# Performance work log

Hardware: AMD Instinct MI355X
Metric: run time of the kernel (lower is better)

## Reference

```python
import jax, jax.numpy as jnp
import numpy as np
import math

NO, NR, E = 100000, 1000, 1000000
DO, DR, DE, H, OM = 64, 32, 4, 64, 32


def setup_inputs() -> dict:
    key = jax.random.key(0)
    ks = jax.random.split(key, 20)
    s = lambda k, sh: jax.random.normal(k, sh, dtype=jnp.float32) * 0.05
    inp = {
        'x_order': jax.random.normal(ks[0], (NO, DO), dtype=jnp.float32),
        'x_rider': jax.random.normal(ks[1], (NR, DR), dtype=jnp.float32),
        'edge_attr': jax.random.normal(ks[2], (E, DE), dtype=jnp.float32),
        'order_idx': jax.random.randint(ks[3], (E,), 0, NO),
        'rider_idx': jax.random.randint(ks[4], (E,), 0, NR),
        'omega_encoded': jax.random.normal(ks[5], (OM,), dtype=jnp.float32),
        # TransformerConv params (heads=1)
        'Wk': s(ks[6], (DO, H)), 'bk': jnp.zeros((H,), jnp.float32),
        'Wq': s(ks[7], (DR, H)), 'bq': jnp.zeros((H,), jnp.float32),
        'Wv': s(ks[8], (DO, H)), 'bv': jnp.zeros((H,), jnp.float32),
        'We': s(ks[9], (DE, H)),  # lin_edge, bias=False in PyG
        'Wskip': s(ks[10], (DR, H)), 'bskip': jnp.zeros((H,), jnp.float32),
        # order_proj
        'Wp': s(ks[11], (DO, H)), 'bp': jnp.zeros((H,), jnp.float32),
        # residual MLP: Linear(2H+OM,128) -> ReLU -> Linear(128,1)
        'W1': s(ks[12], (2 * H + OM, 128)), 'b1': jnp.zeros((128,), jnp.float32),
        'W2': s(ks[13], (128, 1)), 'b2': jnp.zeros((1,), jnp.float32),
    }
    return inp


def _segment_softmax(alpha, seg, num_segments):
    m = jax.ops.segment_max(alpha, seg, num_segments=num_segments)
    m = jnp.where(jnp.isfinite(m), m, 0.0)
    ex = jnp.exp(alpha - m[seg])
    denom = jax.ops.segment_sum(ex, seg, num_segments=num_segments)
    return ex / (denom[seg] + 1e-16)


def reference(x_order, x_rider, edge_attr, order_idx, rider_idx, omega_encoded,
              Wk, bk, Wq, bq, Wv, bv, We, Wskip, bskip, Wp, bp, W1, b1, W2, b2):
    scale = 1.0 / math.sqrt(H)
    # TransformerConv((order, rider) -> rider), heads=1, edge_dim
    q = x_rider @ Wq + bq            # [NR, H]
    k = x_order @ Wk + bk            # [NO, H]
    v = x_order @ Wv + bv            # [NO, H]
    e = edge_attr @ We               # [E, H]
    k_j = k[order_idx] + e           # [E, H]
    v_j = v[order_idx] + e           # [E, H]
    alpha = jnp.sum(q[rider_idx] * k_j, axis=-1) * scale  # [E]
    alpha = _segment_softmax(alpha, rider_idx, NR)
    agg = jax.ops.segment_sum(alpha[:, None] * v_j, rider_idx, num_segments=NR)  # [NR, H]
    rider_emb = agg + x_rider @ Wskip + bskip  # root/skip connection

    # edge scoring
    order_proj = x_order @ Wp + bp   # [NO, H]
    oe = order_proj[order_idx]       # [E, H]
    re = rider_emb[rider_idx]        # [E, H]
    dot = jnp.sum(oe * re, axis=-1) * scale  # [E]
    omega_expand = jnp.broadcast_to(omega_encoded[None, :], (oe.shape[0], OM))
    resid_in = jnp.concatenate([oe, re, omega_expand], axis=-1)  # [E, 2H+OM]
    hmid = jax.nn.relu(resid_in @ W1 + b1)
    resid = (hmid @ W2 + b2)[:, 0]
    return jnp.clip(dot + resid, -10.0, 10.0)
```

## Files before the change

kernel.cpp:

```cpp
#include <hip/hip_runtime.h>
#include <hip/hip_bf16.h>
#include <math.h>

#define NO_N 100000
#define NR_N 1000
#define E_N  1000000
#define SB     250
#define SCHUNK 4000
#define KVP_TILES 1563
#define KVP_BLKS 521
#define MAXTILES 17008

typedef short bf16x8 __attribute__((ext_vector_type(8)));
typedef float floatx4 __attribute__((ext_vector_type(4)));

__device__ __forceinline__ unsigned short bfu(float x) {
    union { __hip_bfloat16 h; unsigned short u; } c;
    c.h = __float2bfloat16(x);
    return c.u;
}
__device__ __forceinline__ float bflo(unsigned int u) {
    return __uint_as_float(u << 16);
}
__device__ __forceinline__ float bfhi(unsigned int u) {
    return __uint_as_float(u & 0xffff0000u);
}

__global__ __launch_bounds__(256) void k_front(
    const float* __restrict__ xr,
    const float* __restrict__ Wq, const float* __restrict__ bq,
    const float* __restrict__ Wskip, const float* __restrict__ bskip,
    const float* __restrict__ We,
    float* __restrict__ q, float* __restrict__ skip, float* __restrict__ t,
    const float* __restrict__ W1, const float* __restrict__ b1,
    const float* __restrict__ omega, float* __restrict__ b1eff,
    const float* __restrict__ x,
    const float* __restrict__ Wk, const float* __restrict__ bk,
    const float* __restrict__ Wv, const float* __restrict__ bv,
    const float* __restrict__ Wp, const float* __restrict__ bp,
    unsigned short* __restrict__ kb, unsigned short* __restrict__ vb,
    unsigned short* __restrict__ pb,
    const int* __restrict__ ridx, int* __restrict__ ghist)
{
    __shared__ __align__(16) char smem[9216];
    const int tid = threadIdx.x;
    const int b = blockIdx.x;

    if (b < 250) {
        float* sx = (float*)smem;
        float* sq = sx + 128;
        int rbase = b * 4;
        if (tid < 128) {
            int rl = tid >> 5, d = tid & 31;
            sx[rl * 32 + d] = xr[(rbase + rl) * 32 + d];
        }
        __syncthreads();
        int rl = tid >> 6, h = tid & 63;
        int r = rbase + rl;
        float aq = bq[h], as = bskip[h];
        #pragma unroll 4
        for (int d = 0; d < 32; ++d) {
            float xv = sx[rl * 32 + d];
            aq += xv * Wq[d * 64 + h];
            as += xv * Wskip[d * 64 + h];
        }
        sq[rl * 64 + h] = aq;
        q[r * 64 + h] = aq;
        skip[r * 64 + h] = as;
        __syncthreads();
        if (tid < 16) {
            int rl2 = tid >> 2, d = tid & 3;
            float acc = 0.f;
            for (int hh = 0; hh < 64; ++hh)
                acc += We[d * 64 + hh] * sq[rl2 * 64 + hh];
            t[(rbase + rl2) * 4 + d] = acc;
        }
    } else if (b == 250) {
        if (tid < 128) {
            float acc = b1[tid];
            #pragma unroll 4
            for (int j = 0; j < 32; ++j)
                acc += omega[j] * W1[(128 + j) * 128 + tid];
            b1eff[tid] = acc;
        }
    } else if (b < 251 + KVP_BLKS) {
        unsigned short* sX = (unsigned short*)smem;
        const int wave = tid >> 6, lane = tid & 63;
        const int l15 = lane & 15, quad = lane >> 4;

        bf16x8 bfr[3][2];
        float bias[3];
        unsigned short* outT[3];
        int colc[3];
        #pragma unroll
        for (int ct = 0; ct < 3; ++ct) {
            int n = wave * 48 + ct * 16 + l15;
            int table = n >> 6, c = n & 63;
            const float* W  = (table == 0) ? Wk : (table == 1) ? Wv : Wp;
            const float* bb = (table == 0) ? bk : (table == 1) ? bv : bp;
            bias[ct] = bb[c];
            colc[ct] = c;
            outT[ct] = (table == 0) ? kb : (table == 1) ? vb : pb;
            #pragma unroll
            for (int kf = 0; kf < 2; ++kf) {
                bf16x8 f;
                #pragma unroll
                for (int j = 0; j < 8; ++j)
                    f[j] = (short)bfu(W[(size_t)(kf * 32 + quad * 8 + j) * 64 + c]);
                bfr[ct][kf] = f;
            }
        }

        const int srl = tid >> 2;
        const int sqt = (tid & 3) * 16;

        for (int tile = b - 251; tile < KVP_TILES; tile += KVP_BLKS) {
            int rowbase = tile * 64;
            {
                int row = rowbase + srl;
                unsigned short* dst = sX + srl * 72 + sqt;
                if (row < NO_N) {
                    const float4* src = (const float4*)(x + (size_t)row * 64 + sqt);
                    #pragma unroll
                    for (int i = 0; i < 4; ++i) {
                        float4 a = src[i];
                        ushort4 u = { bfu(a.x), bfu(a.y), bfu(a.z), bfu(a.w) };
                        *(ushort4*)(dst + i * 4) = u;
                    }
                } else {
                    ushort4 z = {0, 0, 0, 0};
                    #pragma unroll
                    for (int i = 0; i < 4; ++i) *(ushort4*)(dst + i * 4) = z;
                }
            }
            __syncthreads();

            floatx4 acc[4][3];
            #pragma unroll
            for (int rt = 0; rt < 4; ++rt)
                #pragma unroll
                for (int ct = 0; ct < 3; ++ct)
                    acc[rt][ct] = (floatx4){bias[ct], bias[ct], bias[ct], bias[ct]};

            #pragma unroll
            for (int rt = 0; rt < 4; ++rt) {
                const unsigned short* ar = sX + (size_t)(rt * 16 + l15) * 72 + quad * 8;
                bf16x8 a0 = *(const bf16x8*)(ar);
                bf16x8 a1 = *(const bf16x8*)(ar + 32);
                #pragma unroll
                for (int ct = 0; ct < 3; ++ct) {
                    floatx4 c = acc[rt][ct];
                    c = __builtin_amdgcn_mfma_f32_16x16x32_bf16(a0, bfr[ct][0], c, 0, 0, 0);
                    c = __builtin_amdgcn_mfma_f32_16x16x32_bf16(a1, bfr[ct][1], c, 0, 0, 0);
                    acc[rt][ct] = c;
                }
            }

            #pragma unroll
            for (int rt = 0; rt < 4; ++rt) {
                int rb = rowbase + rt * 16 + quad * 4;
                #pragma unroll
                for (int ct = 0; ct < 3; ++ct) {
                    unsigned short* o = outT[ct];
                    size_t cbase = colc[ct];
                    #pragma unroll
                    for (int g = 0; g < 4; ++g) {
                        int row = rb + g;
                        if (row < NO_N)
                            o[(size_t)row * 64 + cbase] = bfu(acc[rt][ct][g]);
                    }
                }
            }
            __syncthreads();
        }
    } else {
        int* hc = (int*)smem;
        int hb = b - (251 + KVP_BLKS);
        for (int i = tid; i < NR_N; i += 256) hc[i] = 0;
        __syncthreads();
        int s = hb * SCHUNK;
        for (int i = s + tid; i < s + SCHUNK; i += 256)
            atomicAdd(&hc[ridx[i]], 1);
        __syncthreads();
        for (int i = tid; i < NR_N; i += 256)
            ghist[i * SB + hb] = hc[i];
    }
}

__global__ __launch_bounds__(256) void k_colscan(const int* __restrict__ ghist,
                                                 int* __restrict__ gpre,
                                                 int* __restrict__ counts)
{
    __shared__ int s[256];
    int tid = threadIdx.x, r = blockIdx.x;
    int v = (tid < SB) ? ghist[r * SB + tid] : 0;
    s[tid] = v;
    __syncthreads();
    for (int off = 1; off < 256; off <<= 1) {
        int tv = (tid >= off) ? s[tid - off] : 0;
        __syncthreads();
        s[tid] += tv;
        __syncthreads();
    }
    if (tid < SB) gpre[r * SB + tid] = s[tid] - v;
    if (tid == 255) counts[r] = s[255];
}

__global__ __launch_bounds__(1024) void k_scan(const int* __restrict__ counts,
                                               int* __restrict__ offsets,
                                               int* __restrict__ tilestart,
                                               int* __restrict__ tile2r)
{
    __shared__ int s[1024];
    int tid = threadIdx.x;
    int c = (tid < NR_N) ? counts[tid] : 0;
    s[tid] = c;
    __syncthreads();
    for (int off = 1; off < 1024; off <<= 1) {
        int tv = (tid >= off) ? s[tid - off] : 0;
        __syncthreads();
        s[tid] += tv;
        __syncthreads();
    }
    if (tid < NR_N) offsets[tid] = s[tid] - c;
    if (tid == NR_N - 1) offsets[NR_N] = s[tid];
    __syncthreads();
    int tc = (tid < NR_N) ? ((c + 63) >> 6) : 0;
    s[tid] = tc;
    __syncthreads();
    for (int off = 1; off < 1024; off <<= 1) {
        int tv = (tid >= off) ? s[tid - off] : 0;
        __syncthreads();
        s[tid] += tv;
        __syncthreads();
    }
    if (tid < NR_N) {
        int ts = s[tid] - tc;
        tilestart[tid] = ts;
        for (int t = 0; t < tc; ++t) tile2r[ts + t] = tid;
    }
    if (tid == NR_N - 1) tilestart[NR_N] = s[tid];
}

__global__ __launch_bounds__(256) void k_scatter2(
    const int* __restrict__ ridx, const int* __restrict__ oidx,
    const float* __restrict__ ea, const float* __restrict__ t,
    const int* __restrict__ offsets, const int* __restrict__ gpre,
    int4* __restrict__ spack, int* __restrict__ so, int* __restrict__ rank)
{
    __shared__ int cur[NR_N];
    int tid = threadIdx.x, b = blockIdx.x;
    for (int i = tid; i < NR_N; i += 256)
        cur[i] = offsets[i] + gpre[i * SB + b];
    __syncthreads();
    int s = b * SCHUNK;
    for (int i = s + tid; i < s + SCHUNK; i += 256) {
        int r = ridx[i];
        int o = oidx[i];
        float4 e4 = *(const float4*)(ea + (size_t)i * 4);
        float4 t4 = *(const float4*)(t + r * 4);
        float h = e4.x * t4.x + e4.y * t4.y + e4.z * t4.z + e4.w * t4.w;
        int pos = atomicAdd(&cur[r], 1);
        int4 pk;
        pk.x = o;
        pk.y = __float_as_int(h);
        pk.z = (int)((unsigned)bfu(e4.x) | ((unsigned)bfu(e4.y) << 16));
        pk.w = (int)((unsigned)bfu(e4.z) | ((unsigned)bfu(e4.w) << 16));
        spack[pos] = pk;
        so[pos] = o;
        rank[i] = pos;
    }
}

__global__ __launch_bounds__(1024) void k_rider(
    const int* __restrict__ offsets, const int4* __restrict__ spack,
    const float* __restrict__ q,
    const unsigned short* __restrict__ kb, const unsigned short* __restrict__ vb,
    const float* __restrict__ We, const float* __restrict__ skip,
    const float* __restrict__ W1, const float* __restrict__ b1eff,
    float* __restrict__ emb, float* __restrict__ Br)
{
    __shared__ float sQ[64];
    __shared__ int2 sOX[16][64];
    __shared__ float rv[16][64];
    __shared__ float re4[16][4];
    __shared__ float rd[16];

    int r = blockIdx.x;
    int wave = threadIdx.x >> 6, lane = threadIdx.x & 63;
    if (threadIdx.x < 64) sQ[threadIdx.x] = q[r * 64 + threadIdx.x];
    __syncthreads();

    int beg = offsets[r], end = offsets[r + 1];
    int cnt = end - beg;
    int chunk = (cnt + 15) >> 4;
    int s0 = beg + wave * chunk;
    int s1 = min(s0 + chunk, end);

    float aggv = 0.f, dsum = 0.f;
    float ag0 = 0.f, ag1 = 0.f, ag2 = 0.f, ag3 = 0.f;
    const float2* sQ2 = (const float2*)sQ;

    for (int jb = s0; jb < s1; jb += 64) {
        int j = jb + lane;
        bool valid = (j < s1);
        int4 pk = make_int4(0, 0, 0, 0);
        if (valid) pk = spack[j];
        int oo = pk.x;
        float h = __int_as_float(pk.y);

        const uint4* krow = (const uint4*)(kb + (size_t)oo * 64);
        uint4 K0 = krow[0], K1 = krow[1], K2 = krow[2], K3 = krow[3];
        uint4 K4 = krow[4], K5 = krow[5], K6 = krow[6], K7 = krow[7];
        float acc = h;
        #define DOT8(Kv, base) { \
            float2 qa = sQ2[(base) + 0]; \
            acc = fmaf(bflo(Kv.x), qa.x, acc); acc = fmaf(bfhi(Kv.x), qa.y, acc); \
            float2 qb = sQ2[(base) + 1]; \
            acc = fmaf(bflo(Kv.y), qb.x, acc); acc = fmaf(bfhi(Kv.y), qb.y, acc); \
            float2 qc = sQ2[(base) + 2]; \
            acc = fmaf(bflo(Kv.z), qc.x, acc); acc = fmaf(bfhi(Kv.z), qc.y, acc); \
            float2 qd = sQ2[(base) + 3]; \
            acc = fmaf(bflo(Kv.w), qd.x, acc); acc = fmaf(bfhi(Kv.w), qd.y, acc); }
        DOT8(K0, 0) DOT8(K1, 4) DOT8(K2, 8) DOT8(K3, 12)
        DOT8(K4, 16) DOT8(K5, 20) DOT8(K6, 24) DOT8(K7, 28)
        #undef DOT8

        float exv = valid ? __expf(acc * 0.125f) : 0.f;
        dsum += exv;
        unsigned int ez = (unsigned int)pk.z, ew = (unsigned int)pk.w;
        ag0 = fmaf(exv, bflo(ez), ag0);
        ag1 = fmaf(exv, bfhi(ez), ag1);
        ag2 = fmaf(exv, bflo(ew), ag2);
        ag3 = fmaf(exv, bfhi(ew), ag3);

        sOX[wave][lane] = make_int2(oo, __float_as_int(exv));

        int nn = min(s1 - jb, 64);
        int i = 0;
        for (; i + 8 <= nn; i += 8) {
            int2 x0 = sOX[wave][i + 0], x1 = sOX[wave][i + 1];
            int2 x2 = sOX[wave][i + 2], x3 = sOX[wave][i + 3];
            int2 x4 = sOX[wave][i + 4], x5 = sOX[wave][i + 5];
            int2 x6 = sOX[wave][i + 6], x7 = sOX[wave][i + 7];
            unsigned short u0 = vb[(size_t)x0.x * 64 + lane];
            unsigned short u1 = vb[(size_t)x1.x * 64 + lane];
            unsigned short u2 = vb[(size_t)x2.x * 64 + lane];
            unsigned short u3 = vb[(size_t)x3.x * 64 + lane];
            unsigned short u4 = vb[(size_t)x4.x * 64 + lane];
            unsigned short u5 = vb[(size_t)x5.x * 64 + lane];
            unsigned short u6 = vb[(size_t)x6.x * 64 + lane];
            unsigned short u7 = vb[(size_t)x7.x * 64 + lane];
            aggv = fmaf(__int_as_float(x0.y), __uint_as_float((unsigned int)u0 << 16), aggv);
            aggv = fmaf(__int_as_float(x1.y), __uint_as_float((unsigned int)u1 << 16), aggv);
            aggv = fmaf(__int_as_float(x2.y), __uint_as_float((unsigned int)u2 << 16), aggv);
            aggv = fmaf(__int_as_float(x3.y), __uint_as_float((unsigned int)u3 << 16), aggv);
            aggv = fmaf(__int_as_float(x4.y), __uint_as_float((unsigned int)u4 << 16), aggv);
            aggv = fmaf(__int_as_float(x5.y), __uint_as_float((unsigned int)u5 << 16), aggv);
            aggv = fmaf(__int_as_float(x6.y), __uint_as_float((unsigned int)u6 << 16), aggv);
            aggv = fmaf(__int_as_float(x7.y), __uint_as_float((unsigned int)u7 << 16), aggv);
        }
        for (; i < nn; ++i) {
            int2 xx = sOX[wave][i];
            unsigned short uu = vb[(size_t)xx.x * 64 + lane];
            aggv = fmaf(__int_as_float(xx.y), __uint_as_float((unsigned int)uu << 16), aggv);
        }
    }

    #pragma unroll
    for (int m = 1; m < 64; m <<= 1) {
        dsum += __shfl_xor(dsum, m);
        ag0 += __shfl_xor(ag0, m);
        ag1 += __shfl_xor(ag1, m);
        ag2 += __shfl_xor(ag2, m);
        ag3 += __shfl_xor(ag3, m);
    }

    rv[wave][lane] = aggv;
    if (lane == 0) {
        rd[wave] = dsum;
        re4[wave][0] = ag0; re4[wave][1] = ag1;
        re4[wave][2] = ag2; re4[wave][3] = ag3;
    }
    __syncthreads();
    if (threadIdx.x < 64) {
        int l = threadIdx.x;
        float av = 0.f, ds = 0.f, a0 = 0.f, a1 = 0.f, a2 = 0.f, a3 = 0.f;
        #pragma unroll 4
        for (int w = 0; w < 16; ++w) {
            av += rv[w][l]; ds += rd[w];
            a0 += re4[w][0]; a1 += re4[w][1]; a2 += re4[w][2]; a3 += re4[w][3];
        }
        float corr = a0 * We[0 * 64 + l] + a1 * We[1 * 64 + l]
                   + a2 * We[2 * 64 + l] + a3 * We[3 * 64 + l];
        float val = (av + corr) / (ds + 1e-16f) + skip[r * 64 + l];
        emb[r * 64 + l] = val;
        sQ[l] = val;
    }
    __syncthreads();
    if (threadIdx.x < 128) {
        int c = threadIdx.x;
        float a = b1eff[c];
        #pragma unroll 8
        for (int d = 0; d < 64; ++d)
            a = fmaf(sQ[d], W1[(size_t)(64 + d) * 128 + c], a);
        Br[r * 128 + c] = a;
    }
}

__global__ __launch_bounds__(256, 3) void k_edge2(
    const int* __restrict__ so, const int* __restrict__ offsets,
    const int* __restrict__ tilestart, const int* __restrict__ tile2r,
    const unsigned short* __restrict__ pb, const float* __restrict__ emb,
    const float* __restrict__ Br, const float* __restrict__ W1,
    const float* __restrict__ W2, const float* __restrict__ b2,
    float* __restrict__ tmp)
{
    __shared__ __align__(16) unsigned short sA[64 * 72];
    __shared__ float sDot[64];

    const int tid = threadIdx.x;
    const int wave = tid >> 6;
    const int lane = tid & 63;
    const int l15 = lane & 15;
    const int quad = lane >> 4;

    bf16x8 bfr[8][2];
    float w2v[8];
    #pragma unroll
    for (int ctl = 0; ctl < 8; ++ctl) {
        int n = ctl * 16 + l15;
        w2v[ctl] = W2[n];
        #pragma unroll
        for (int kc = 0; kc < 2; ++kc) {
            bf16x8 f;
            #pragma unroll
            for (int j = 0; j < 8; ++j)
                f[j] = (short)bfu(W1[(size_t)(kc * 32 + quad * 8 + j) * 128 + n]);
            bfr[ctl][kc] = f;
        }
    }
    float b2v = b2[0];
    const int ntiles = tilestart[NR_N];

    const int el = tid >> 2;
    const int q16 = (tid & 3) * 16;

    for (int tile = blockIdx.x; tile < ntiles; tile += gridDim.x) {
        int r = tile2r[tile];
        int jb = offsets[r] + ((tile - tilestart[r]) << 6);
        int jend = offsets[r + 1];

        {
            int j = jb + el;
            int o = so[min(j, jend - 1)];
            const uint4* po = (const uint4*)(pb + (size_t)o * 64 + q16);
            uint4 A0 = po[0], A1 = po[1];
            const float4* pe = (const float4*)(emb + r * 64 + q16);
            float4 e0 = pe[0], e1 = pe[1], e2 = pe[2], e3 = pe[3];
            float dotp;
            dotp  = bflo(A0.x) * e0.x + bfhi(A0.x) * e0.y;
            dotp += bflo(A0.y) * e0.z + bfhi(A0.y) * e0.w;
            dotp += bflo(A0.z) * e1.x + bfhi(A0.z) * e1.y;
            dotp += bflo(A0.w) * e1.z + bfhi(A0.w) * e1.w;
            dotp += bflo(A1.x) * e2.x + bfhi(A1.x) * e2.y;
            dotp += bflo(A1.y) * e2.z + bfhi(A1.y) * e2.w;
            dotp += bflo(A1.z) * e3.x + bfhi(A1.z) * e3.y;
            dotp += bflo(A1.w) * e3.z + bfhi(A1.w) * e3.w;
            uint4* sp = (uint4*)(sA + el * 72 + q16);
            sp[0] = A0; sp[1] = A1;
            dotp += __shfl_xor(dotp, 1);
            dotp += __shfl_xor(dotp, 2);
            if ((tid & 3) == 0) sDot[el] = dotp;
        }

        const unsigned short* ar = sA + (size_t)(wave * 16 + l15) * 72 + quad * 8;
        bf16x8 a0 = *(const bf16x8*)(ar);
        bf16x8 a1 = *(const bf16x8*)(ar + 32);
        floatx4 acc[8];
        #pragma unroll
        for (int ctl = 0; ctl < 8; ++ctl) {
            floatx4 c = (floatx4){0.f, 0.f, 0.f, 0.f};
            c = __builtin_amdgcn_mfma_f32_16x16x32_bf16(a0, bfr[ctl][0], c, 0, 0, 0);
            c = __builtin_amdgcn_mfma_f32_16x16x32_bf16(a1, bfr[ctl][1], c, 0, 0, 0);
            acc[ctl] = c;
        }

        float brv[8];
        #pragma unroll
        for (int ctl = 0; ctl < 8; ++ctl)
            brv[ctl] = Br[r * 128 + ctl * 16 + l15];

        floatx4 s;
        #pragma unroll
        for (int g = 0; g < 4; ++g) {
            float v = 0.f;
            #pragma unroll
            for (int ctl = 0; ctl < 8; ++ctl)
                v = fmaf(fmaxf(acc[ctl][g] + brv[ctl], 0.f), w2v[ctl], v);
            s[g] = v;
        }
        #pragma unroll
        for (int m = 1; m < 16; m <<= 1) {
            s[0] += __shfl_xor(s[0], m);
            s[1] += __shfl_xor(s[1], m);
            s[2] += __shfl_xor(s[2], m);
            s[3] += __shfl_xor(s[3], m);
        }
        if (l15 == 0) {
            int rowb = wave * 16 + quad * 4;
            #pragma unroll
            for (int g = 0; g < 4; ++g) {
                int pos = jb + rowb + g;
                if (pos < jend) {
                    float v = s[g] + 0.125f * sDot[rowb + g] + b2v;
                    tmp[pos] = fminf(fmaxf(v, -10.f), 10.f);
                }
            }
        }
    }
}

__global__ __launch_bounds__(256) void k_perm(const int* __restrict__ rank,
                                              const float* __restrict__ tmp,
                                              float* __restrict__ out)
{
    int i = blockIdx.x * 256 + threadIdx.x;
    if (i < E_N) out[i] = tmp[rank[i]];
}

extern "C" void kernel_launch(void* const* d_in, const int* in_sizes, int n_in,
                              void* d_out, int out_size, void* d_ws, size_t ws_size,
                              hipStream_t stream)
{
    const float* x_order   = (const float*)d_in[0];
    const float* x_rider   = (const float*)d_in[1];
    const float* edge_attr = (const float*)d_in[2];
    const int*   order_idx = (const int*)d_in[3];
    const int*   rider_idx = (const int*)d_in[4];
    const float* omega     = (const float*)d_in[5];
    const float* Wk = (const float*)d_in[6];  const float* bk = (const float*)d_in[7];
    const float* Wq = (const float*)d_in[8];  const float* bq = (const float*)d_in[9];
    const float* Wv = (const float*)d_in[10]; const float* bv = (const float*)d_in[11];
    const float* We = (const float*)d_in[12];
    const float* Wskip = (const float*)d_in[13]; const float* bskip = (const float*)d_in[14];
    const float* Wp = (const float*)d_in[15]; const float* bp = (const float*)d_in[16];
    const float* W1 = (const float*)d_in[17]; const float* b1 = (const float*)d_in[18];
    const float* W2 = (const float*)d_in[19]; const float* b2 = (const float*)d_in[20];
    float* out = (float*)d_out;

    unsigned short* ws_kb = (unsigned short*)d_ws;
    unsigned short* ws_vb = ws_kb + (size_t)NO_N * 64;
    unsigned short* ws_pb = ws_vb + (size_t)NO_N * 64;
    int4* ws_spack = (int4*)(ws_pb + (size_t)NO_N * 64);
    float* ws_tmp  = (float*)ws_spack;
    int*  ws_so    = (int*)(ws_spack + E_N);
    int*  ws_rank  = ws_so + E_N;
    float* wsf     = (float*)(ws_rank + E_N);
    float* ws_q    = wsf;
    float* ws_skip = ws_q + NR_N * 64;
    float* ws_emb  = ws_skip + NR_N * 64;
    float* ws_t    = ws_emb + NR_N * 64;
    float* ws_b1e  = ws_t + NR_N * 4;
    float* ws_Br   = ws_b1e + 128;
    int* ws_counts  = (int*)(ws_Br + NR_N * 128);
    int* ws_offsets = ws_counts + NR_N;
    int* ws_tilest  = ws_offsets + NR_N + 8;
    int* ws_tile2r  = ws_tilest + NR_N + 8;
    int* ws_ghist   = ws_tile2r + MAXTILES;
    int* ws_gpre    = ws_ghist + NR_N * SB;

    k_front<<<251 + KVP_BLKS + SB, 256, 0, stream>>>(
        x_rider, Wq, bq, Wskip, bskip, We, ws_q, ws_skip, ws_t,
        W1, b1, omega, ws_b1e,
        x_order, Wk, bk, Wv, bv, Wp, bp, ws_kb, ws_vb, ws_pb,
        rider_idx, ws_ghist);
    k_colscan<<<NR_N, 256, 0, stream>>>(ws_ghist, ws_gpre, ws_counts);
    k_scan<<<1, 1024, 0, stream>>>(ws_counts, ws_offsets, ws_tilest, ws_tile2r);
    k_scatter2<<<SB, 256, 0, stream>>>(rider_idx, order_idx, edge_attr, ws_t,
                                       ws_offsets, ws_gpre, ws_spack, ws_so, ws_rank);
    k_rider<<<NR_N, 1024, 0, stream>>>(ws_offsets, ws_spack, ws_q,
                                       ws_kb, ws_vb, We, ws_skip,
                                       W1, ws_b1e, ws_emb, ws_Br);
    k_edge2<<<2048, 256, 0, stream>>>(ws_so, ws_offsets, ws_tilest, ws_tile2r,
                                      ws_pb, ws_emb, ws_Br, W1, W2, b2, ws_tmp);
    k_perm<<<(E_N + 255) / 256, 256, 0, stream>>>(ws_rank, ws_tmp, out);
}
```

Measured before the change: 312.6 us.

## Prefetch next edge tile's gathers in k_edge2 and use contiguous tile ranges

k_edge2 now gives each block a contiguous range of tiles instead of a grid-strided loop. While the current tile is being computed, it issues the next tile's tile2r/offsets lookups and the gather of projected order rows, so gather latency overlaps the MFMA work. The Br bias load is moved ahead of the MFMAs. The edge grid doubles to 4096 blocks and KVP_BLKS rises to 1024, which changes the k_front launch split. The cost is extra registers for the double-buffered rows, and with only a few tiles per block the prefetch has little room to hide latency.

```diff
diff --git a/kernel.cpp b/kernel.cpp
--- a/kernel.cpp
+++ b/kernel.cpp
@@ -8,7 +8,7 @@
 #define SB     250
 #define SCHUNK 4000
 #define KVP_TILES 1563
-#define KVP_BLKS 521
+#define KVP_BLKS 1024
 #define MAXTILES 17008
 
 typedef short bf16x8 __attribute__((ext_vector_type(8)));
@@ -442,37 +442,58 @@
     }
     float b2v = b2[0];
     const int ntiles = tilestart[NR_N];
+    int tpb = (ntiles + gridDim.x - 1) / gridDim.x;
+    int t0 = blockIdx.x * tpb;
+    int t1 = min(t0 + tpb, ntiles);
+    if (t0 >= t1) return;
 
     const int el = tid >> 2;
     const int q16 = (tid & 3) * 16;
 
-    for (int tile = blockIdx.x; tile < ntiles; tile += gridDim.x) {
-        int r = tile2r[tile];
-        int jb = offsets[r] + ((tile - tilestart[r]) << 6);
-        int jend = offsets[r + 1];
+    int r = tile2r[t0];
+    int jb = offsets[r] + ((t0 - tilestart[r]) << 6);
+    int jend = offsets[r + 1];
+    int o = so[min(jb + el, jend - 1)];
+    const uint4* po = (const uint4*)(pb + (size_t)o * 64 + q16);
+    uint4 A0 = po[0], A1 = po[1];
+
+    for (int tile = t0; tile < t1; ++tile) {
+        const int cr = r, cjb = jb, cjend = jend;
+        const uint4 cA0 = A0, cA1 = A1;
+
+        int nt = tile + 1;
+        if (nt < t1) {
+            r = tile2r[nt];
+            jb = offsets[r] + ((nt - tilestart[r]) << 6);
+            jend = offsets[r + 1];
+            int on = so[min(jb + el, jend - 1)];
+            const uint4* pn = (const uint4*)(pb + (size_t)on * 64 + q16);
+            A0 = pn[0]; A1 = pn[1];
+        }
 
         {
-            int j = jb + el;
-            int o = so[min(j, jend - 1)];
-            const uint4* po = (const uint4*)(pb + (size_t)o * 64 + q16);
-            uint4 A0 = po[0], A1 = po[1];
-            const float4* pe = (const float4*)(emb + r * 64 + q16);
+            const float4* pe = (const float4*)(emb + cr * 64 + q16);
             float4 e0 = pe[0], e1 = pe[1], e2 = pe[2], e3 = pe[3];
             float dotp;
-            dotp  = bflo(A0.x) * e0.x + bfhi(A0.x) * e0.y;
-            dotp += bflo(A0.y) * e0.z + bfhi(A0.y) * e0.w;
-            dotp += bflo(A0.z) * e1.x + bfhi(A0.z) * e1.y;
-            dotp += bflo(A0.w) * e1.z + bfhi(A0.w) * e1.w;
-            dotp += bflo(A1.x) * e2.x + bfhi(A1.x) * e2.y;
-            dotp += bflo(A1.y) * e2.z + bfhi(A1.y) * e2.w;
-            dotp += bflo(A1.z) * e3.x + bfhi(A1.z) * e3.y;
-            dotp += bflo(A1.w) * e3.z + bfhi(A1.w) * e3.w;
+            dotp  = bflo(cA0.x) * e0.x + bfhi(cA0.x) * e0.y;
+            dotp += bflo(cA0.y) * e0.z + bfhi(cA0.y) * e0.w;
+            dotp += bflo(cA0.z) * e1.x + bfhi(cA0.z) * e1.y;
+            dotp += bflo(cA0.w) * e1.z + bfhi(cA0.w) * e1.w;
+            dotp += bflo(cA1.x) * e2.x + bfhi(cA1.x) * e2.y;
+            dotp += bflo(cA1.y) * e2.z + bfhi(cA1.y) * e2.w;
+            dotp += bflo(cA1.z) * e3.x + bfhi(cA1.z) * e3.y;
+            dotp += bflo(cA1.w) * e3.z + bfhi(cA1.w) * e3.w;
             uint4* sp = (uint4*)(sA + el * 72 + q16);
-            sp[0] = A0; sp[1] = A1;
+            sp[0] = cA0; sp[1] = cA1;
             dotp += __shfl_xor(dotp, 1);
             dotp += __shfl_xor(dotp, 2);
             if ((tid & 3) == 0) sDot[el] = dotp;
         }
+
+        float brv[8];
+        #pragma unroll
+        for (int ctl = 0; ctl < 8; ++ctl)
+            brv[ctl] = Br[cr * 128 + ctl * 16 + l15];
 
         const unsigned short* ar = sA + (size_t)(wave * 16 + l15) * 72 + quad * 8;
         bf16x8 a0 = *(const bf16x8*)(ar);
@@ -486,11 +507,6 @@
             acc[ctl] = c;
         }
 
-        float brv[8];
-        #pragma unroll
-        for (int ctl = 0; ctl < 8; ++ctl)
-            brv[ctl] = Br[r * 128 + ctl * 16 + l15];
-
         floatx4 s;
         #pragma unroll
         for (int g = 0; g < 4; ++g) {
@@ -511,8 +527,8 @@
             int rowb = wave * 16 + quad * 4;
             #pragma unroll
             for (int g = 0; g < 4; ++g) {
-                int pos = jb + rowb + g;
-                if (pos < jend) {
+                int pos = cjb + rowb + g;
+                if (pos < cjend) {
                     float v = s[g] + 0.125f * sDot[rowb + g] + b2v;
                     tmp[pos] = fminf(fmaxf(v, -10.f), 10.f);
                 }
@@ -582,7 +598,7 @@
     k_rider<<<NR_N, 1024, 0, stream>>>(ws_offsets, ws_spack, ws_q,
                                        ws_kb, ws_vb, We, ws_skip,
                                        W1, ws_b1e, ws_emb, ws_Br);
-    k_edge2<<<2048, 256, 0, stream>>>(ws_so, ws_offsets, ws_tilest, ws_tile2r,
+    k_edge2<<<4096, 256, 0, stream>>>(ws_so, ws_offsets, ws_tilest, ws_tile2r,
                                       ws_pb, ws_emb, ws_Br, W1, W2, b2, ws_tmp);
     k_perm<<<(E_N + 255) / 256, 256, 0, stream>>>(ws_rank, ws_tmp, out);
 }
```

Result: no change. 315.3 us (+0.9%).

## Process tile pairs with early gathers, precomputed tile records, and fused epilogue

Applied to the files above, without the earlier changes.

The edge-scoring kernel now handles two tiles per iteration and issues both tiles' gathers of order projections up front, so the second tile's memory latency overlaps the first tile's MFMA work. A precomputed int4 tile record (rider, start, end) replaces the chained tile2r/offsets/tilestart lookups. The ReLU/W2 epilogue is folded into the MFMA loop so the 8 accumulator vectors no longer stay live, and the KVP block count in the front kernel increases. In exchange it uses more registers and doubles the shared buffers, which may hurt occupancy at the 3-blocks-per-SM bound.

```diff
diff --git a/kernel.cpp b/kernel.cpp
--- a/kernel.cpp
+++ b/kernel.cpp
@@ -1,6 +1,7 @@
 #include <hip/hip_runtime.h>
 #include <hip/hip_bf16.h>
 #include <math.h>
+#include <stdint.h>
 
 #define NO_N 100000
 #define NR_N 1000
@@ -8,7 +9,7 @@
 #define SB     250
 #define SCHUNK 4000
 #define KVP_TILES 1563
-#define KVP_BLKS 521
+#define KVP_BLKS 1024
 #define MAXTILES 17008
 
 typedef short bf16x8 __attribute__((ext_vector_type(8)));
@@ -209,7 +210,7 @@
 __global__ __launch_bounds__(1024) void k_scan(const int* __restrict__ counts,
                                                int* __restrict__ offsets,
                                                int* __restrict__ tilestart,
-                                               int* __restrict__ tile2r)
+                                               int4* __restrict__ trec)
 {
     __shared__ int s[1024];
     int tid = threadIdx.x;
@@ -222,7 +223,8 @@
         s[tid] += tv;
         __syncthreads();
     }
-    if (tid < NR_N) offsets[tid] = s[tid] - c;
+    int off0 = s[tid] - c;
+    if (tid < NR_N) offsets[tid] = off0;
     if (tid == NR_N - 1) offsets[NR_N] = s[tid];
     __syncthreads();
     int tc = (tid < NR_N) ? ((c + 63) >> 6) : 0;
@@ -237,7 +239,9 @@
     if (tid < NR_N) {
         int ts = s[tid] - tc;
         tilestart[tid] = ts;
-        for (int t = 0; t < tc; ++t) tile2r[ts + t] = tid;
+        int jend = off0 + c;
+        for (int t = 0; t < tc; ++t)
+            trec[ts + t] = make_int4(tid, off0 + (t << 6), jend, 0);
     }
     if (tid == NR_N - 1) tilestart[NR_N] = s[tid];
 }
@@ -409,15 +413,15 @@
 }
 
 __global__ __launch_bounds__(256, 3) void k_edge2(
-    const int* __restrict__ so, const int* __restrict__ offsets,
-    const int* __restrict__ tilestart, const int* __restrict__ tile2r,
+    const int* __restrict__ so, const int4* __restrict__ trec,
+    const int* __restrict__ tilestart,
     const unsigned short* __restrict__ pb, const float* __restrict__ emb,
     const float* __restrict__ Br, const float* __restrict__ W1,
     const float* __restrict__ W2, const float* __restrict__ b2,
     float* __restrict__ tmp)
 {
-    __shared__ __align__(16) unsigned short sA[64 * 72];
-    __shared__ float sDot[64];
+    __shared__ __align__(16) unsigned short sA[2][64 * 72];
+    __shared__ float sDot[2][64];
 
     const int tid = threadIdx.x;
     const int wave = tid >> 6;
@@ -442,21 +446,26 @@
     }
     float b2v = b2[0];
     const int ntiles = tilestart[NR_N];
+    const int npairs = (ntiles + 1) >> 1;
 
     const int el = tid >> 2;
     const int q16 = (tid & 3) * 16;
 
-    for (int tile = blockIdx.x; tile < ntiles; tile += gridDim.x) {
-        int r = tile2r[tile];
-        int jb = offsets[r] + ((tile - tilestart[r]) << 6);
-        int jend = offsets[r + 1];
+    for (int p = blockIdx.x; p < npairs; p += gridDim.x) {
+        int tA = p * 2, tB = tA + 1;
+        bool hasB = (tB < ntiles);
+        int4 ra = trec[tA];
+        int4 rb = hasB ? trec[tB] : ra;
+
+        int oA = so[min(ra.y + el, ra.z - 1)];
+        const uint4* pA = (const uint4*)(pb + (size_t)oA * 64 + q16);
+        uint4 A0 = pA[0], A1 = pA[1];
+        int oB = so[min(rb.y + el, rb.z - 1)];
+        const uint4* pB = (const uint4*)(pb + (size_t)oB * 64 + q16);
+        uint4 B0 = pB[0], B1 = pB[1];
 
         {
-            int j = jb + el;
-            int o = so[min(j, jend - 1)];
-            const uint4* po = (const uint4*)(pb + (size_t)o * 64 + q16);
-            uint4 A0 = po[0], A1 = po[1];
-            const float4* pe = (const float4*)(emb + r * 64 + q16);
+            const float4* pe = (const float4*)(emb + ra.x * 64 + q16);
             float4 e0 = pe[0], e1 = pe[1], e2 = pe[2], e3 = pe[3];
             float dotp;
             dotp  = bflo(A0.x) * e0.x + bfhi(A0.x) * e0.y;
@@ -467,54 +476,104 @@
             dotp += bflo(A1.y) * e2.z + bfhi(A1.y) * e2.w;
             dotp += bflo(A1.z) * e3.x + bfhi(A1.z) * e3.y;
             dotp += bflo(A1.w) * e3.z + bfhi(A1.w) * e3.w;
-            uint4* sp = (uint4*)(sA + el * 72 + q16);
+            uint4* sp = (uint4*)(&sA[0][el * 72 + q16]);
             sp[0] = A0; sp[1] = A1;
             dotp += __shfl_xor(dotp, 1);
             dotp += __shfl_xor(dotp, 2);
-            if ((tid & 3) == 0) sDot[el] = dotp;
-        }
-
-        const unsigned short* ar = sA + (size_t)(wave * 16 + l15) * 72 + quad * 8;
-        bf16x8 a0 = *(const bf16x8*)(ar);
-        bf16x8 a1 = *(const bf16x8*)(ar + 32);
-        floatx4 acc[8];
-        #pragma unroll
-        for (int ctl = 0; ctl < 8; ++ctl) {
-            floatx4 c = (floatx4){0.f, 0.f, 0.f, 0.f};
-            c = __builtin_amdgcn_mfma_f32_16x16x32_bf16(a0, bfr[ctl][0], c, 0, 0, 0);
-            c = __builtin_amdgcn_mfma_f32_16x16x32_bf16(a1, bfr[ctl][1], c, 0, 0, 0);
-            acc[ctl] = c;
-        }
-
-        float brv[8];
-        #pragma unroll
-        for (int ctl = 0; ctl < 8; ++ctl)
-            brv[ctl] = Br[r * 128 + ctl * 16 + l15];
-
-        floatx4 s;
-        #pragma unroll
-        for (int g = 0; g < 4; ++g) {
-            float v = 0.f;
+            if ((tid & 3) == 0) sDot[0][el] = dotp;
+        }
+        {
+            float brv[8];
             #pragma unroll
             for (int ctl = 0; ctl < 8; ++ctl)
-                v = fmaf(fmaxf(acc[ctl][g] + brv[ctl], 0.f), w2v[ctl], v);
-            s[g] = v;
-        }
-        #pragma unroll
-        for (int m = 1; m < 16; m <<= 1) {
-            s[0] += __shfl_xor(s[0], m);
-            s[1] += __shfl_xor(s[1], m);
-            s[2] += __shfl_xor(s[2], m);
-            s[3] += __shfl_xor(s[3], m);
-        }
-        if (l15 == 0) {
-            int rowb = wave * 16 + quad * 4;
-            #pragma unroll
-            for (int g = 0; g < 4; ++g) {
-                int pos = jb + rowb + g;
-                if (pos < jend) {
-                    float v = s[g] + 0.125f * sDot[rowb + g] + b2v;
-                    tmp[pos] = fminf(fmaxf(v, -10.f), 10.f);
+                brv[ctl] = Br[ra.x * 128 + ctl * 16 + l15];
+
+            const unsigned short* ar = &sA[0][(wave * 16 + l15) * 72 + quad * 8];
+            bf16x8 a0 = *(const bf16x8*)(ar);
+            bf16x8 a1 = *(const bf16x8*)(ar + 32);
+            floatx4 s = (floatx4){0.f, 0.f, 0.f, 0.f};
+            #pragma unroll
+            for (int ctl = 0; ctl < 8; ++ctl) {
+                floatx4 c = (floatx4){0.f, 0.f, 0.f, 0.f};
+                c = __builtin_amdgcn_mfma_f32_16x16x32_bf16(a0, bfr[ctl][0], c, 0, 0, 0);
+                c = __builtin_amdgcn_mfma_f32_16x16x32_bf16(a1, bfr[ctl][1], c, 0, 0, 0);
+                #pragma unroll
+                for (int g = 0; g < 4; ++g)
+                    s[g] = fmaf(fmaxf(c[g] + brv[ctl], 0.f), w2v[ctl], s[g]);
+            }
+            #pragma unroll
+            for (int m = 1; m < 16; m <<= 1) {
+                s[0] += __shfl_xor(s[0], m);
+                s[1] += __shfl_xor(s[1], m);
+                s[2] += __shfl_xor(s[2], m);
+                s[3] += __shfl_xor(s[3], m);
+            }
+            if (l15 == 0) {
+                int rowb = wave * 16 + quad * 4;
+                #pragma unroll
+                for (int g = 0; g < 4; ++g) {
+                    int pos = ra.y + rowb + g;
+                    if (pos < ra.z) {
+                        float v = s[g] + 0.125f * sDot[0][rowb + g] + b2v;
+                        tmp[pos] = fminf(fmaxf(v, -10.f), 10.f);
+                    }
+                }
+            }
+        }
+
+        if (hasB) {
+            {
+                const float4* pe = (const float4*)(emb + rb.x * 64 + q16);
+                float4 e0 = pe[0], e1 = pe[1], e2 = pe[2], e3 = pe[3];
+                float dotp;
+                dotp  = bflo(B0.x) * e0.x + bfhi(B0.x) * e0.y;
+                dotp += bflo(B0.y) * e0.z + bfhi(B0.y) * e0.w;
+                dotp += bflo(B0.z) * e1.x + bfhi(B0.z) * e1.y;
+                dotp += bflo(B0.w) * e1.z + bfhi(B0.w) * e1.w;
+                dotp += bflo(B1.x) * e2.x + bfhi(B1.x) * e2.y;
+                dotp += bflo(B1.y) * e2.z + bfhi(B1.y) * e2.w;
+                dotp += bflo(B1.z) * e3.x + bfhi(B1.z) * e3.y;
+                dotp += bflo(B1.w) * e3.z + bfhi(B1.w) * e3.w;
+                uint4* sp = (uint4*)(&sA[1][el * 72 + q16]);
+                sp[0] = B0; sp[1] = B1;
+                dotp += __shfl_xor(dotp, 1);
+                dotp += __shfl_xor(dotp, 2);
+                if ((tid & 3) == 0) sDot[1][el] = dotp;
+            }
+            float brv[8];
+            #pragma unroll
+            for (int ctl = 0; ctl < 8; ++ctl)
+                brv[ctl] = Br[rb.x * 128 + ctl * 16 + l15];
+
+            const unsigned short* ar = &sA[1][(wave * 16 + l15) * 72 + quad * 8];
+            bf16x8 a0 = *(const bf16x8*)(ar);
+            bf16x8 a1 = *(const bf16x8*)(ar + 32);
+            floatx4 s = (floatx4){0.f, 0.f, 0.f, 0.f};
+            #pragma unroll
+            for (int ctl = 0; ctl < 8; ++ctl) {
+                floatx4 c = (floatx4){0.f, 0.f, 0.f, 0.f};
+                c = __builtin_amdgcn_mfma_f32_16x16x32_bf16(a0, bfr[ctl][0], c, 0, 0, 0);
+                c = __builtin_amdgcn_mfma_f32_16x16x32_bf16(a1, bfr[ctl][1], c, 0, 0, 0);
+                #pragma unroll
+                for (int g = 0; g < 4; ++g)
+                    s[g] = fmaf(fmaxf(c[g] + brv[ctl], 0.f), w2v[ctl], s[g]);
+            }
+            #pragma unroll
+            for (int m = 1; m < 16; m <<= 1) {
+                s[0] += __shfl_xor(s[0], m);
+                s[1] += __shfl_xor(s[1], m);
+                s[2] += __shfl_xor(s[2], m);
+                s[3] += __shfl_xor(s[3], m);
+            }
+            if (l15 == 0) {
+                int rowb = wave * 16 + quad * 4;
+                #pragma unroll
+                for (int g = 0; g < 4; ++g) {
+                    int pos = rb.y + rowb + g;
+                    if (pos < rb.z) {
+                        float v = s[g] + 0.125f * sDot[1][rowb + g] + b2v;
+                        tmp[pos] = fminf(fmaxf(v, -10.f), 10.f);
+                    }
                 }
             }
         }
@@ -566,9 +625,9 @@
     int* ws_counts  = (int*)(ws_Br + NR_N * 128);
     int* ws_offsets = ws_counts + NR_N;
     int* ws_tilest  = ws_offsets + NR_N + 8;
-    int* ws_tile2r  = ws_tilest + NR_N + 8;
-    int* ws_ghist   = ws_tile2r + MAXTILES;
+    int* ws_ghist   = ws_tilest + NR_N + 8;
     int* ws_gpre    = ws_ghist + NR_N * SB;
+    int4* ws_trec   = (int4*)(((uintptr_t)(ws_gpre + NR_N * SB) + 15) & ~(uintptr_t)15);
 
     k_front<<<251 + KVP_BLKS + SB, 256, 0, stream>>>(
         x_rider, Wq, bq, Wskip, bskip, We, ws_q, ws_skip, ws_t,
@@ -576,13 +635,13 @@
         x_order, Wk, bk, Wv, bv, Wp, bp, ws_kb, ws_vb, ws_pb,
         rider_idx, ws_ghist);
     k_colscan<<<NR_N, 256, 0, stream>>>(ws_ghist, ws_gpre, ws_counts);
-    k_scan<<<1, 1024, 0, stream>>>(ws_counts, ws_offsets, ws_tilest, ws_tile2r);
+    k_scan<<<1, 1024, 0, stream>>>(ws_counts, ws_offsets, ws_tilest, ws_trec);
     k_scatter2<<<SB, 256, 0, stream>>>(rider_idx, order_idx, edge_attr, ws_t,
                                        ws_offsets, ws_gpre, ws_spack, ws_so, ws_rank);
     k_rider<<<NR_N, 1024, 0, stream>>>(ws_offsets, ws_spack, ws_q,
                                        ws_kb, ws_vb, We, ws_skip,
                                        W1, ws_b1e, ws_emb, ws_Br);
-    k_edge2<<<2048, 256, 0, stream>>>(ws_so, ws_offsets, ws_tilest, ws_tile2r,
+    k_edge2<<<2048, 256, 0, stream>>>(ws_so, ws_trec, ws_tilest,
                                       ws_pb, ws_emb, ws_Br, W1, W2, b2, ws_tmp);
     k_perm<<<(E_N + 255) / 256, 256, 0, stream>>>(ws_rank, ws_tmp, out);
 }
```

New measurement: 315.7 us. About the same (+1.0%).

## Batch four tiles per edge-scoring block with prefetched gathers and tile records

Applied to the files above, without the earlier changes.

The edge scoring kernel now processes groups of four 64-edge tiles per block iteration. It issues all order-row gathers for the group up front so their memory latency overlaps, and it folds the ReLU/W2 reduction into the MFMA loop to drop the 8-accumulator array. The scan kernel now emits per-tile records (rider, start, end) so the edge kernel avoids dependent lookups through tile2r and offsets. Separately, k_rider drops to 512 threads with 8 waves, the k_edge2 grid grows to 4096 blocks without the occupancy hint, and the k_front projection block count rises. The cost is more registers held for prefetched rows, which may lower occupancy.

```diff
diff --git a/kernel.cpp b/kernel.cpp
--- a/kernel.cpp
+++ b/kernel.cpp
@@ -1,6 +1,7 @@
 #include <hip/hip_runtime.h>
 #include <hip/hip_bf16.h>
 #include <math.h>
+#include <stdint.h>
 
 #define NO_N 100000
 #define NR_N 1000
@@ -8,7 +9,7 @@
 #define SB     250
 #define SCHUNK 4000
 #define KVP_TILES 1563
-#define KVP_BLKS 521
+#define KVP_BLKS 1024
 #define MAXTILES 17008
 
 typedef short bf16x8 __attribute__((ext_vector_type(8)));
@@ -209,7 +210,7 @@
 __global__ __launch_bounds__(1024) void k_scan(const int* __restrict__ counts,
                                                int* __restrict__ offsets,
                                                int* __restrict__ tilestart,
-                                               int* __restrict__ tile2r)
+                                               int4* __restrict__ trec)
 {
     __shared__ int s[1024];
     int tid = threadIdx.x;
@@ -222,7 +223,8 @@
         s[tid] += tv;
         __syncthreads();
     }
-    if (tid < NR_N) offsets[tid] = s[tid] - c;
+    int off0 = s[tid] - c;
+    if (tid < NR_N) offsets[tid] = off0;
     if (tid == NR_N - 1) offsets[NR_N] = s[tid];
     __syncthreads();
     int tc = (tid < NR_N) ? ((c + 63) >> 6) : 0;
@@ -237,7 +239,9 @@
     if (tid < NR_N) {
         int ts = s[tid] - tc;
         tilestart[tid] = ts;
-        for (int t = 0; t < tc; ++t) tile2r[ts + t] = tid;
+        int jend = off0 + c;
+        for (int t = 0; t < tc; ++t)
+            trec[ts + t] = make_int4(tid, off0 + (t << 6), jend, 0);
     }
     if (tid == NR_N - 1) tilestart[NR_N] = s[tid];
 }
@@ -272,7 +276,7 @@
     }
 }
 
-__global__ __launch_bounds__(1024) void k_rider(
+__global__ __launch_bounds__(512) void k_rider(
     const int* __restrict__ offsets, const int4* __restrict__ spack,
     const float* __restrict__ q,
     const unsigned short* __restrict__ kb, const unsigned short* __restrict__ vb,
@@ -281,10 +285,10 @@
     float* __restrict__ emb, float* __restrict__ Br)
 {
     __shared__ float sQ[64];
-    __shared__ int2 sOX[16][64];
-    __shared__ float rv[16][64];
-    __shared__ float re4[16][4];
-    __shared__ float rd[16];
+    __shared__ int2 sOX[8][64];
+    __shared__ float rv[8][64];
+    __shared__ float re4[8][4];
+    __shared__ float rd[8];
 
     int r = blockIdx.x;
     int wave = threadIdx.x >> 6, lane = threadIdx.x & 63;
@@ -293,7 +297,7 @@
 
     int beg = offsets[r], end = offsets[r + 1];
     int cnt = end - beg;
-    int chunk = (cnt + 15) >> 4;
+    int chunk = (cnt + 7) >> 3;
     int s0 = beg + wave * chunk;
     int s1 = min(s0 + chunk, end);
 
@@ -386,8 +390,8 @@
     if (threadIdx.x < 64) {
         int l = threadIdx.x;
         float av = 0.f, ds = 0.f, a0 = 0.f, a1 = 0.f, a2 = 0.f, a3 = 0.f;
-        #pragma unroll 4
-        for (int w = 0; w < 16; ++w) {
+        #pragma unroll
+        for (int w = 0; w < 8; ++w) {
             av += rv[w][l]; ds += rd[w];
             a0 += re4[w][0]; a1 += re4[w][1]; a2 += re4[w][2]; a3 += re4[w][3];
         }
@@ -408,9 +412,9 @@
     }
 }
 
-__global__ __launch_bounds__(256, 3) void k_edge2(
-    const int* __restrict__ so, const int* __restrict__ offsets,
-    const int* __restrict__ tilestart, const int* __restrict__ tile2r,
+__global__ __launch_bounds__(256) void k_edge2(
+    const int* __restrict__ so, const int4* __restrict__ trec,
+    const int* __restrict__ tilestart,
     const unsigned short* __restrict__ pb, const float* __restrict__ emb,
     const float* __restrict__ Br, const float* __restrict__ W1,
     const float* __restrict__ W2, const float* __restrict__ b2,
@@ -442,79 +446,81 @@
     }
     float b2v = b2[0];
     const int ntiles = tilestart[NR_N];
+    const int ngrp = (ntiles + 3) >> 2;
 
     const int el = tid >> 2;
     const int q16 = (tid & 3) * 16;
 
-    for (int tile = blockIdx.x; tile < ntiles; tile += gridDim.x) {
-        int r = tile2r[tile];
-        int jb = offsets[r] + ((tile - tilestart[r]) << 6);
-        int jend = offsets[r + 1];
-
-        {
-            int j = jb + el;
-            int o = so[min(j, jend - 1)];
-            const uint4* po = (const uint4*)(pb + (size_t)o * 64 + q16);
-            uint4 A0 = po[0], A1 = po[1];
-            const float4* pe = (const float4*)(emb + r * 64 + q16);
-            float4 e0 = pe[0], e1 = pe[1], e2 = pe[2], e3 = pe[3];
-            float dotp;
-            dotp  = bflo(A0.x) * e0.x + bfhi(A0.x) * e0.y;
-            dotp += bflo(A0.y) * e0.z + bfhi(A0.y) * e0.w;
-            dotp += bflo(A0.z) * e1.x + bfhi(A0.z) * e1.y;
-            dotp += bflo(A0.w) * e1.z + bfhi(A0.w) * e1.w;
-            dotp += bflo(A1.x) * e2.x + bfhi(A1.x) * e2.y;
-            dotp += bflo(A1.y) * e2.z + bfhi(A1.y) * e2.w;
-            dotp += bflo(A1.z) * e3.x + bfhi(A1.z) * e3.y;
-            dotp += bflo(A1.w) * e3.z + bfhi(A1.w) * e3.w;
-            uint4* sp = (uint4*)(sA + el * 72 + q16);
-            sp[0] = A0; sp[1] = A1;
-            dotp += __shfl_xor(dotp, 1);
-            dotp += __shfl_xor(dotp, 2);
-            if ((tid & 3) == 0) sDot[el] = dotp;
-        }
-
-        const unsigned short* ar = sA + (size_t)(wave * 16 + l15) * 72 + quad * 8;
-        bf16x8 a0 = *(const bf16x8*)(ar);
-        bf16x8 a1 = *(const bf16x8*)(ar + 32);
-        floatx4 acc[8];
+    for (int g = blockIdx.x; g < ngrp; g += gridDim.x) {
+        int tb = g * 4;
+        int4 rr[4];
+        uint4 P0[4], P1[4];
+
         #pragma unroll
-        for (int ctl = 0; ctl < 8; ++ctl) {
-            floatx4 c = (floatx4){0.f, 0.f, 0.f, 0.f};
-            c = __builtin_amdgcn_mfma_f32_16x16x32_bf16(a0, bfr[ctl][0], c, 0, 0, 0);
-            c = __builtin_amdgcn_mfma_f32_16x16x32_bf16(a1, bfr[ctl][1], c, 0, 0, 0);
-            acc[ctl] = c;
-        }
-
-        float brv[8];
+        for (int i = 0; i < 4; ++i)
+            rr[i] = trec[min(tb + i, ntiles - 1)];
         #pragma unroll
-        for (int ctl = 0; ctl < 8; ++ctl)
-            brv[ctl] = Br[r * 128 + ctl * 16 + l15];
-
-        floatx4 s;
+        for (int i = 0; i < 4; ++i) {
+            int o = so[min(rr[i].y + el, rr[i].z - 1)];
+            const uint4* p = (const uint4*)(pb + (size_t)o * 64 + q16);
+            P0[i] = p[0];
+            P1[i] = p[1];
+        }
+
         #pragma unroll
-        for (int g = 0; g < 4; ++g) {
-            float v = 0.f;
+        for (int i = 0; i < 4; ++i) {
+            {
+                const float4* pe = (const float4*)(emb + rr[i].x * 64 + q16);
+                float4 e0 = pe[0], e1 = pe[1], e2 = pe[2], e3 = pe[3];
+                float dotp;
+                dotp  = bflo(P0[i].x) * e0.x + bfhi(P0[i].x) * e0.y;
+                dotp += bflo(P0[i].y) * e0.z + bfhi(P0[i].y) * e0.w;
+                dotp += bflo(P0[i].z) * e1.x + bfhi(P0[i].z) * e1.y;
+                dotp += bflo(P0[i].w) * e1.z + bfhi(P0[i].w) * e1.w;
+                dotp += bflo(P1[i].x) * e2.x + bfhi(P1[i].x) * e2.y;
+                dotp += bflo(P1[i].y) * e2.z + bfhi(P1[i].y) * e2.w;
+                dotp += bflo(P1[i].z) * e3.x + bfhi(P1[i].z) * e3.y;
+                dotp += bflo(P1[i].w) * e3.z + bfhi(P1[i].w) * e3.w;
+                uint4* sp = (uint4*)(sA + el * 72 + q16);
+                sp[0] = P0[i]; sp[1] = P1[i];
+                dotp += __shfl_xor(dotp, 1);
+                dotp += __shfl_xor(dotp, 2);
+                if ((tid & 3) == 0) sDot[el] = dotp;
+            }
+            float brv[8];
             #pragma unroll
             for (int ctl = 0; ctl < 8; ++ctl)
-                v = fmaf(fmaxf(acc[ctl][g] + brv[ctl], 0.f), w2v[ctl], v);
-            s[g] = v;
-        }
-        #pragma unroll
-        for (int m = 1; m < 16; m <<= 1) {
-            s[0] += __shfl_xor(s[0], m);
-            s[1] += __shfl_xor(s[1], m);
-            s[2] += __shfl_xor(s[2], m);
-            s[3] += __shfl_xor(s[3], m);
-        }
-        if (l15 == 0) {
-            int rowb = wave * 16 + quad * 4;
-            #pragma unroll
-            for (int g = 0; g < 4; ++g) {
-                int pos = jb + rowb + g;
-                if (pos < jend) {
-                    float v = s[g] + 0.125f * sDot[rowb + g] + b2v;
-                    tmp[pos] = fminf(fmaxf(v, -10.f), 10.f);
+                brv[ctl] = Br[rr[i].x * 128 + ctl * 16 + l15];
+
+            const unsigned short* ar = sA + (size_t)(wave * 16 + l15) * 72 + quad * 8;
+            bf16x8 a0 = *(const bf16x8*)(ar);
+            bf16x8 a1 = *(const bf16x8*)(ar + 32);
+            floatx4 s = (floatx4){0.f, 0.f, 0.f, 0.f};
+            #pragma unroll
+            for (int ctl = 0; ctl < 8; ++ctl) {
+                floatx4 c = (floatx4){0.f, 0.f, 0.f, 0.f};
+                c = __builtin_amdgcn_mfma_f32_16x16x32_bf16(a0, bfr[ctl][0], c, 0, 0, 0);
+                c = __builtin_amdgcn_mfma_f32_16x16x32_bf16(a1, bfr[ctl][1], c, 0, 0, 0);
+                #pragma unroll
+                for (int gg = 0; gg < 4; ++gg)
+                    s[gg] = fmaf(fmaxf(c[gg] + brv[ctl], 0.f), w2v[ctl], s[gg]);
+            }
+            #pragma unroll
+            for (int m = 1; m < 16; m <<= 1) {
+                s[0] += __shfl_xor(s[0], m);
+                s[1] += __shfl_xor(s[1], m);
+                s[2] += __shfl_xor(s[2], m);
+                s[3] += __shfl_xor(s[3], m);
+            }
+            if (l15 == 0) {
+                int rowb = wave * 16 + quad * 4;
+                #pragma unroll
+                for (int gg = 0; gg < 4; ++gg) {
+                    int pos = rr[i].y + rowb + gg;
+                    if (pos < rr[i].z) {
+                        float v = s[gg] + 0.125f * sDot[rowb + gg] + b2v;
+                        tmp[pos] = fminf(fmaxf(v, -10.f), 10.f);
+                    }
                 }
             }
         }
@@ -566,9 +572,9 @@
     int* ws_counts  = (int*)(ws_Br + NR_N * 128);
     int* ws_offsets = ws_counts + NR_N;
     int* ws_tilest  = ws_offsets + NR_N + 8;
-    int* ws_tile2r  = ws_tilest + NR_N + 8;
-    int* ws_ghist   = ws_tile2r + MAXTILES;
+    int* ws_ghist   = ws_tilest + NR_N + 8;
     int* ws_gpre    = ws_ghist + NR_N * SB;
+    int4* ws_trec   = (int4*)(((uintptr_t)(ws_gpre + NR_N * SB) + 15) & ~(uintptr_t)15);
 
     k_front<<<251 + KVP_BLKS + SB, 256, 0, stream>>>(
         x_rider, Wq, bq, Wskip, bskip, We, ws_q, ws_skip, ws_t,
@@ -576,13 +582,13 @@
         x_order, Wk, bk, Wv, bv, Wp, bp, ws_kb, ws_vb, ws_pb,
         rider_idx, ws_ghist);
     k_colscan<<<NR_N, 256, 0, stream>>>(ws_ghist, ws_gpre, ws_counts);
-    k_scan<<<1, 1024, 0, stream>>>(ws_counts, ws_offsets, ws_tilest, ws_tile2r);
+    k_scan<<<1, 1024, 0, stream>>>(ws_counts, ws_offsets, ws_tilest, ws_trec);
     k_scatter2<<<SB, 256, 0, stream>>>(rider_idx, order_idx, edge_attr, ws_t,
                                        ws_offsets, ws_gpre, ws_spack, ws_so, ws_rank);
-    k_rider<<<NR_N, 1024, 0, stream>>>(ws_offsets, ws_spack, ws_q,
-                                       ws_kb, ws_vb, We, ws_skip,
-                                       W1, ws_b1e, ws_emb, ws_Br);
-    k_edge2<<<2048, 256, 0, stream>>>(ws_so, ws_offsets, ws_tilest, ws_tile2r,
+    k_rider<<<NR_N, 512, 0, stream>>>(ws_offsets, ws_spack, ws_q,
+                                      ws_kb, ws_vb, We, ws_skip,
+                                      W1, ws_b1e, ws_emb, ws_Br);
+    k_edge2<<<4096, 256, 0, stream>>>(ws_so, ws_trec, ws_tilest,
                                       ws_pb, ws_emb, ws_Br, W1, W2, b2, ws_tmp);
     k_perm<<<(E_N + 255) / 256, 256, 0, stream>>>(ws_rank, ws_tmp, out);
 }
```

Result: no change. 315.4 us (+0.9%).
